# Kernel optimization log

Hardware: AMD Instinct MI355X
Metric: run time of the kernel (lower is better)

The kernel has to match this reference:

```python
import jax, jax.numpy as jnp
import numpy as np

B, N, C = 16, 65536, 21          # batch, anchors, classes (class 0 = background)
TH_CONF = 0.05                   # confidence threshold
TH_IOU = 0.5                     # NMS IoU threshold
TOP_K = 200                      # candidates kept per (batch, class) before NMS
V0, V1 = 0.1, 0.2                # SSD box-coder variances


def setup_inputs() -> dict:
    key = jax.random.key(0)
    k1, k2, k3, k4 = jax.random.split(key, 4)
    conf = jax.random.normal(k1, (B, N, C), dtype=jnp.float32)
    loc = jax.random.normal(k2, (B, N, 4), dtype=jnp.float32)
    # anchors in center form (cx, cy, w, h), normalized coords
    cxcy = jax.random.uniform(k3, (N, 2), dtype=jnp.float32)
    wh = 0.02 + 0.2 * jax.random.uniform(k4, (N, 2), dtype=jnp.float32)
    anchors = jnp.concatenate([cxcy, wh], axis=-1)
    return {"conf": conf, "loc": loc, "anchors": anchors}


def _decode(anchors, loc):
    # SSD decode: anchors [N,4] center form, loc [B,N,4] offsets -> [B,N,4] xyxy
    a_xy, a_wh = anchors[:, :2], anchors[:, 2:]
    xy = a_xy + loc[..., :2] * V0 * a_wh
    wh = a_wh * jnp.exp(loc[..., 2:] * V1)
    return jnp.concatenate([xy - 0.5 * wh, xy + 0.5 * wh], axis=-1)


def _iou(boxes):
    # boxes [K,4] xyxy -> pairwise IoU [K,K]
    area = jnp.maximum(boxes[:, 2] - boxes[:, 0], 0.0) * jnp.maximum(boxes[:, 3] - boxes[:, 1], 0.0)
    lt = jnp.maximum(boxes[:, None, :2], boxes[None, :, :2])
    rb = jnp.minimum(boxes[:, None, 2:], boxes[None, :, 2:])
    wh = jnp.maximum(rb - lt, 0.0)
    inter = wh[..., 0] * wh[..., 1]
    union = area[:, None] + area[None, :] - inter
    return inter / jnp.maximum(union, 1e-9)


def _nms_keep(iou, valid):
    # greedy NMS over score-sorted candidates; valid = (score >= TH_CONF)
    K = iou.shape[0]
    idx = jnp.arange(K)

    def body(keep, xs):
        row, v, i = xs
        suppressed = jnp.any((row > TH_IOU) & keep & (idx < i))
        k = v & (~suppressed)
        return keep.at[i].set(k), 0

    keep, _ = jax.lax.scan(body, jnp.zeros((K,), dtype=bool), (iou, valid, idx))
    return keep


def reference(conf, loc, anchors):
    score = jax.nn.softmax(conf, axis=2)            # [B,N,C]
    boxes = _decode(anchors, loc)                   # [B,N,4]
    # skip background class 0 (cls_base = 1 for softmax classifier)
    cls_scores = jnp.swapaxes(score[..., 1:], 1, 2)  # [B,C-1,N]
    top_s, top_i = jax.lax.top_k(cls_scores, TOP_K)  # [B,C-1,K], sorted desc
    top_boxes = jax.vmap(lambda bx, ix: bx[ix])(boxes, top_i)  # [B,C-1,K,4]
    valid = top_s >= TH_CONF
    keep = jax.vmap(jax.vmap(lambda b, v: _nms_keep(_iou(b), v)))(top_boxes, valid)  # [B,C-1,K]
    out_boxes = jnp.where(keep[..., None], top_boxes, 0.0)
    out_scores = jnp.where(keep, top_s, 0.0)
    return jnp.concatenate([out_boxes, out_scores[..., None]], axis=-1)  # [B,C-1,K,5]
```

## Files before the change

### kernel.cpp

```cpp
#include <hip/hip_runtime.h>
#include <stdint.h>

#define NB     16
#define NANCH  65536
#define NC     21
#define NCLS   20
#define NCOL   (NB * NCLS)
#define TOPK   200
#define NBINS  1024
#define CAP    256
#define CAPCOL 4096
#define CAPFAST 2048
#define CNTSTRIDE 16

constexpr float TH      = 0.05f;
constexpr float TPRE    = 0.20f;
constexpr float SCALE20 = (float)NBINS / 0.80f;
constexpr float SCALE05 = (float)NBINS / 0.95f;

__device__ __forceinline__ int bin20(float s) {
  int b = (int)((s - 0.20f) * SCALE20);
  return b < 0 ? 0 : (b > NBINS - 1 ? NBINS - 1 : b);
}
__device__ __forceinline__ int bin05(float s) {
  int b = (int)((s - 0.05f) * SCALE05);
  return b < 0 ? 0 : (b > NBINS - 1 ? NBINS - 1 : b);
}

__device__ __forceinline__ unsigned long long shflx64(unsigned long long v, int m) {
  unsigned int lo = (unsigned int)v, hi = (unsigned int)(v >> 32);
  lo = __shfl_xor(lo, m);
  hi = __shfl_xor(hi, m);
  return ((unsigned long long)hi << 32) | lo;
}
__device__ __forceinline__ unsigned long long rl64(unsigned long long v, int lane) {
  unsigned int lo = __builtin_amdgcn_readlane((int)(unsigned int)v, lane);
  unsigned int hi = __builtin_amdgcn_readlane((int)(unsigned int)(v >> 32), lane);
  return ((unsigned long long)hi << 32) | lo;
}

__device__ __forceinline__ void softmax_tail(const float* x, float* e, float& S) {
  float m = x[0];
#pragma unroll
  for (int c = 1; c < NC; ++c) m = fmaxf(m, x[c]);
#pragma unroll
  for (int c = 0; c < NC; ++c) e[c] = expf(x[c] - m);
  float r0 = e[0] + e[8],  r1 = e[1] + e[9],  r2 = e[2] + e[10], r3 = e[3] + e[11];
  float r4 = e[4] + e[12], r5 = e[5] + e[13], r6 = e[6] + e[14], r7 = e[7] + e[15];
  S = ((r0 + r1) + (r2 + r3)) + ((r4 + r5) + (r6 + r7));
  S += e[16]; S += e[17]; S += e[18]; S += e[19]; S += e[20];
}

__global__ __launch_bounds__(256) void softmax_collect_kernel(
    const float* __restrict__ conf,
    unsigned int* __restrict__ cnt, unsigned long long* __restrict__ cand) {
  const int tid = threadIdx.x;
  __shared__ float ld[256 * NC];
  const float4* src = (const float4*)conf + (long long)blockIdx.x * 1344;
  float4* dst4 = (float4*)ld;
#pragma unroll
  for (int i = 0; i < 5; ++i) dst4[tid + i * 256] = src[tid + i * 256];
  if (tid < 64) dst4[tid + 1280] = src[tid + 1280];
  __syncthreads();

  const int a = blockIdx.x * 256 + tid;
  const int b = a >> 16;
  const int n = a & (NANCH - 1);
  float x[NC];
#pragma unroll
  for (int c = 0; c < NC; ++c) x[c] = ld[tid * NC + c];
  float e[NC], S;
  softmax_tail(x, e, S);
  const float t = TPRE * S;
  unsigned int takemask = 0;
#pragma unroll
  for (int c = 0; c < NCLS; ++c)
    if (e[c + 1] >= t) takemask |= (1u << c);

  __shared__ unsigned int wcnt[4][NCLS];
  __shared__ unsigned int wbase[4][NCLS];
  const int wave = tid >> 6, lane = tid & 63;
#pragma unroll
  for (int c = 0; c < NCLS; ++c) {
    unsigned long long m = __ballot((takemask >> c) & 1);
    if (lane == 0) wcnt[wave][c] = (unsigned int)__popcll(m);
  }
  __syncthreads();
  if (tid < NCLS) {
    const int c = tid;
    unsigned int t0 = wcnt[0][c], t1 = wcnt[1][c], t2 = wcnt[2][c], t3 = wcnt[3][c];
    unsigned int tot = t0 + t1 + t2 + t3;
    unsigned int base = tot ? atomicAdd(&cnt[(b * NCLS + c) * CNTSTRIDE], tot) : 0u;
    wbase[0][c] = base;
    wbase[1][c] = base + t0;
    wbase[2][c] = base + t0 + t1;
    wbase[3][c] = base + t0 + t1 + t2;
  }
  __syncthreads();
#pragma unroll
  for (int c = 0; c < NCLS; ++c) {
    bool take = (takemask >> c) & 1;
    unsigned long long m = __ballot(take);
    if (take) {
      float s = e[c + 1] / S;
      unsigned int off = wbase[wave][c] +
                         (unsigned int)__popcll(m & ((1ULL << lane) - 1));
      if (off < CAPCOL) {
        unsigned int key = __float_as_uint(s) | 0x80000000u;
        cand[(long long)(b * NCLS + c) * CAPCOL + off] =
            ((unsigned long long)(key ^ 0xFFFFFFFFu) << 32) |
            (unsigned long long)(unsigned int)n;
      }
    }
  }
}

__global__ __launch_bounds__(1024) void topk_nms_kernel(
    const unsigned long long* __restrict__ candg,
    const unsigned int* __restrict__ cnt,
    const float* __restrict__ conf, const float* __restrict__ loc,
    const float* __restrict__ anchors, float* __restrict__ out) {
  const int bc = blockIdx.x;
  const int b  = bc / NCLS;
  const int cls = bc % NCLS;
  const int tid = threadIdx.x;

  __shared__ unsigned int hist[NBINS];
  __shared__ unsigned int part[256];
  __shared__ int s_sel, s_n;
  __shared__ unsigned long long cand[CAP];
  __shared__ float4 box4[TOPK];
  __shared__ float sscore[TOPK];
  __shared__ unsigned long long adj[TOPK][4];
  __shared__ unsigned long long keptw[4];

  int nc = (int)cnt[bc * CNTSTRIDE];
  const bool fast = (nc >= TOPK && nc <= CAPFAST);
  for (int i = tid; i < NBINS; i += 1024) hist[i] = 0;
  if (tid == 0) s_n = 0;
  __syncthreads();

  const unsigned long long* cg = candg + (long long)bc * CAPCOL;
  if (fast) {
    for (int i = tid; i < nc; i += 1024) {
      unsigned int key = (unsigned int)(cg[i] >> 32) ^ 0xFFFFFFFFu;
      float s = __uint_as_float(key ^ 0x80000000u);
      atomicAdd(&hist[bin20(s)], 1u);
    }
  } else {
    for (int n = tid; n < NANCH; n += 1024) {
      const float* row = conf + ((long long)b * NANCH + n) * NC;
      float x[NC], e[NC], S;
#pragma unroll
      for (int c = 0; c < NC; ++c) x[c] = row[c];
      softmax_tail(x, e, S);
      float s = e[cls + 1] / S;
      if (s >= TH) atomicAdd(&hist[bin05(s)], 1u);
    }
  }
  __syncthreads();

  if (tid < 256)
    part[tid] = hist[tid*4] + hist[tid*4+1] + hist[tid*4+2] + hist[tid*4+3];
  if (tid == 0) s_sel = -1;
  __syncthreads();
  if (tid < 64) {
    unsigned int p4 = part[tid*4] + part[tid*4+1] + part[tid*4+2] + part[tid*4+3];
    unsigned int sfx = p4;
#pragma unroll
    for (int off = 1; off < 64; off <<= 1) {
      unsigned int o = __shfl_down(sfx, off);
      if (tid + off < 64) sfx += o;
    }
    unsigned int above = sfx - p4;
    if (above < TOPK && sfx >= TOPK) {
      unsigned int cum = above; int sel = tid * 16; bool found = false;
      for (int q = 3; q >= 0 && !found; --q) {
        unsigned int pc = part[tid*4 + q];
        if (cum + pc >= TOPK) {
          for (int i = 3; i >= 0; --i) {
            unsigned int c = hist[(tid*4+q)*4 + i];
            if (cum + c >= TOPK) { sel = (tid*4+q)*4 + i; found = true; break; }
            cum += c;
          }
        } else cum += pc;
      }
      s_sel = sel;
    }
  }
  __syncthreads();
  const int sel = s_sel;

  if (fast) {
    for (int i = tid; i < nc; i += 1024) {
      unsigned long long k64 = cg[i];
      unsigned int key = (unsigned int)(k64 >> 32) ^ 0xFFFFFFFFu;
      float s = __uint_as_float(key ^ 0x80000000u);
      if (bin20(s) >= sel) {
        int pos = atomicAdd(&s_n, 1);
        if (pos < CAP) cand[pos] = k64;
      }
    }
  } else {
    for (int n = tid; n < NANCH; n += 1024) {
      const float* row = conf + ((long long)b * NANCH + n) * NC;
      float x[NC], e[NC], S;
#pragma unroll
      for (int c = 0; c < NC; ++c) x[c] = row[c];
      softmax_tail(x, e, S);
      float s = e[cls + 1] / S;
      if (s >= TH && (sel < 0 || bin05(s) >= sel)) {
        int pos = atomicAdd(&s_n, 1);
        if (pos < CAP) {
          unsigned int key = __float_as_uint(s) | 0x80000000u;
          cand[pos] = ((unsigned long long)(key ^ 0xFFFFFFFFu) << 32) |
                      (unsigned long long)(unsigned int)n;
        }
      }
    }
  }
  __syncthreads();
  int ncand = s_n; if (ncand > CAP) ncand = CAP;

  unsigned long long v = (tid < ncand) ? cand[tid] : ~0ULL;
  for (int k = 2; k <= CAP; k <<= 1) {
    const bool up = ((tid & k) == 0);
    for (int j = k >> 1; j >= 64; j >>= 1) {
      if (tid < 256) cand[tid] = v;
      __syncthreads();
      if (tid < 256) {
        unsigned long long o = cand[tid ^ j];
        bool keepMin = (((tid & j) == 0) == up);
        v = ((v < o) == keepMin) ? v : o;
      }
      __syncthreads();
    }
    if (tid < 256) {
      for (int j = (k >> 1) < 32 ? (k >> 1) : 32; j >= 1; j >>= 1) {
        unsigned long long o = shflx64(v, j);
        bool keepMin = (((tid & j) == 0) == up);
        v = ((v < o) == keepMin) ? v : o;
      }
    }
  }
  const int nsel = (ncand < TOPK) ? ncand : TOPK;

  if (tid < TOPK) {
    if (tid < nsel) {
      unsigned int key = (unsigned int)(v >> 32) ^ 0xFFFFFFFFu;
      float s = __uint_as_float(key ^ 0x80000000u);
      int idx = (int)(unsigned int)(v & 0xFFFFFFFFu);
      float4 anc = ((const float4*)anchors)[idx];
      float4 l   = ((const float4*)loc)[(long long)b * NANCH + idx];
      float cx = anc.x + (l.x * 0.1f) * anc.z;
      float cy = anc.y + (l.y * 0.1f) * anc.w;
      float w  = anc.z * expf(l.z * 0.2f);
      float h  = anc.w * expf(l.w * 0.2f);
      box4[tid] = make_float4(cx - 0.5f * w, cy - 0.5f * h,
                              cx + 0.5f * w, cy + 0.5f * h);
      sscore[tid] = s;
    } else {
      box4[tid] = make_float4(0.f, 0.f, 0.f, 0.f);
      sscore[tid] = 0.0f;
    }
  }
  __syncthreads();

  if (tid < TOPK * 4) {
    const int row = tid >> 2, w = tid & 3;
    const float4 a4 = box4[row];
    const float aar = fmaxf(a4.z - a4.x, 0.f) * fmaxf(a4.w - a4.y, 0.f);
    const int jend = (w < 3) ? 64 : (TOPK - 192);
    unsigned long long roww = 0;
#pragma unroll 4
    for (int jj = 0; jj < jend; ++jj) {
      const int j = (w << 6) + jj;
      float4 b4 = box4[j];
      float jar = fmaxf(b4.z - b4.x, 0.f) * fmaxf(b4.w - b4.y, 0.f);
      float ltx = fmaxf(a4.x, b4.x);
      float lty = fmaxf(a4.y, b4.y);
      float rbx = fminf(a4.z, b4.z);
      float rby = fminf(a4.w, b4.w);
      float iw = fmaxf(rbx - ltx, 0.0f);
      float ih = fmaxf(rby - lty, 0.0f);
      float inter = iw * ih;
      float uni = aar + jar - inter;
      float um = fmaxf(uni, 1e-9f);
      float half = 0.5f * um;
      bool hit;
      if (inter > half * 1.000001f)      hit = true;
      else if (inter < half * 0.999999f) hit = false;
      else                               hit = (inter / um > 0.5f);
      roww |= (unsigned long long)(hit ? 1u : 0u) << jj;
    }
    const int myw = row >> 6, myb = row & 63;
    unsigned long long tri = (w < myw) ? 0ULL
                           : (w > myw) ? ~0ULL
                           : ((myb == 63) ? 0ULL : (~0ULL << (myb + 1)));
    adj[row][w] = roww & tri;
  }
  __syncthreads();

  if (tid < 64) {
    const int l = tid;
    unsigned long long r0[4], r1[4], r2[4], r3[4];
#pragma unroll
    for (int w = 0; w < 4; ++w) {
      r0[w] = adj[l][w];
      r1[w] = adj[l + 64][w];
      r2[w] = adj[l + 128][w];
      r3[w] = (l < 8) ? adj[l + 192][w] : 0ULL;
    }
    unsigned long long sup0 = 0, sup1 = 0, sup2 = 0, sup3 = 0;
    unsigned long long k0 = 0, k1 = 0, k2 = 0, k3 = 0;
#pragma unroll 1
    for (int ii = 0; ii < 64; ++ii) {
      unsigned long long live = ((~sup0 >> ii) & 1ULL) &
                                (unsigned long long)(ii < nsel);
      unsigned long long mask = 0ULL - live;
      k0 |= live << ii;
      sup0 |= rl64(r0[0], ii) & mask; sup1 |= rl64(r0[1], ii) & mask;
      sup2 |= rl64(r0[2], ii) & mask; sup3 |= rl64(r0[3], ii) & mask;
    }
#pragma unroll 1
    for (int ii = 0; ii < 64; ++ii) {
      unsigned long long live = ((~sup1 >> ii) & 1ULL) &
                                (unsigned long long)((64 + ii) < nsel);
      unsigned long long mask = 0ULL - live;
      k1 |= live << ii;
      sup1 |= rl64(r1[1], ii) & mask; sup2 |= rl64(r1[2], ii) & mask;
      sup3 |= rl64(r1[3], ii) & mask;
    }
#pragma unroll 1
    for (int ii = 0; ii < 64; ++ii) {
      unsigned long long live = ((~sup2 >> ii) & 1ULL) &
                                (unsigned long long)((128 + ii) < nsel);
      unsigned long long mask = 0ULL - live;
      k2 |= live << ii;
      sup2 |= rl64(r2[2], ii) & mask; sup3 |= rl64(r2[3], ii) & mask;
    }
#pragma unroll 1
    for (int ii = 0; ii < 8; ++ii) {
      unsigned long long live = ((~sup3 >> ii) & 1ULL) &
                                (unsigned long long)((192 + ii) < nsel);
      unsigned long long mask = 0ULL - live;
      k3 |= live << ii;
      sup3 |= rl64(r3[3], ii) & mask;
    }
    if (l == 0) { keptw[0] = k0; keptw[1] = k1; keptw[2] = k2; keptw[3] = k3; }
  }
  __syncthreads();

  const float* fb = (const float*)box4;
  float* ob = out + (long long)bc * (TOPK * 5);
  for (int pos = tid; pos < TOPK * 5; pos += 1024) {
    int row = pos / 5;
    int k5  = pos - row * 5;
    bool kp = (keptw[row >> 6] >> (row & 63)) & 1ULL;
    float val = (k5 == 4) ? sscore[row] : fb[row * 4 + k5];
    ob[pos] = kp ? val : 0.0f;
  }
}

extern "C" void kernel_launch(void* const* d_in, const int* in_sizes, int n_in,
                              void* d_out, int out_size, void* d_ws, size_t ws_size,
                              hipStream_t stream) {
  const float* conf    = (const float*)d_in[0];
  const float* loc     = (const float*)d_in[1];
  const float* anchors = (const float*)d_in[2];
  float* out = (float*)d_out;

  char* ws = (char*)d_ws;
  unsigned long long* cand = (unsigned long long*)ws;
  unsigned int*       cnt  = (unsigned int*)(ws + 10485760);

  hipMemsetAsync(ws + 10485760, 0, 320 * CNTSTRIDE * 4, stream);
  softmax_collect_kernel<<<(NB * NANCH) / 256, 256, 0, stream>>>(conf, cnt, cand);
  topk_nms_kernel<<<NCOL, 1024, 0, stream>>>(cand, cnt, conf, loc, anchors, out);
}
```

Before: 92.10 us.

## Replace bitonic sort with rank-by-count and use wave-aggregated candidate appends

```diff
diff --git a/kernel.cpp b/kernel.cpp
--- a/kernel.cpp
+++ b/kernel.cpp
@@ -27,12 +27,6 @@
   return b < 0 ? 0 : (b > NBINS - 1 ? NBINS - 1 : b);
 }
 
-__device__ __forceinline__ unsigned long long shflx64(unsigned long long v, int m) {
-  unsigned int lo = (unsigned int)v, hi = (unsigned int)(v >> 32);
-  lo = __shfl_xor(lo, m);
-  hi = __shfl_xor(hi, m);
-  return ((unsigned long long)hi << 32) | lo;
-}
 __device__ __forceinline__ unsigned long long rl64(unsigned long long v, int lane) {
   unsigned int lo = __builtin_amdgcn_readlane((int)(unsigned int)v, lane);
   unsigned int hi = __builtin_amdgcn_readlane((int)(unsigned int)(v >> 32), lane);
@@ -124,6 +118,7 @@
   const int b  = bc / NCLS;
   const int cls = bc % NCLS;
   const int tid = threadIdx.x;
+  const int lane = tid & 63;
 
   __shared__ unsigned int hist[NBINS];
   __shared__ unsigned int part[256];
@@ -137,6 +132,8 @@
   int nc = (int)cnt[bc * CNTSTRIDE];
   const bool fast = (nc >= TOPK && nc <= CAPFAST);
   for (int i = tid; i < NBINS; i += 1024) hist[i] = 0;
+  if (tid < CAP) cand[tid] = ~0ULL;
+  if (tid < TOPK) { box4[tid] = make_float4(0.f,0.f,0.f,0.f); sscore[tid] = 0.f; }
   if (tid == 0) s_n = 0;
   __syncthreads();
 
@@ -192,76 +189,73 @@
   const int sel = s_sel;
 
   if (fast) {
-    for (int i = tid; i < nc; i += 1024) {
-      unsigned long long k64 = cg[i];
-      unsigned int key = (unsigned int)(k64 >> 32) ^ 0xFFFFFFFFu;
-      float s = __uint_as_float(key ^ 0x80000000u);
-      if (bin20(s) >= sel) {
-        int pos = atomicAdd(&s_n, 1);
+    const int ncr = (nc + 1023) & ~1023;
+    for (int i = tid; i < ncr; i += 1024) {
+      bool have = i < nc;
+      unsigned long long k64 = have ? cg[i] : 0ULL;
+      bool takeit = false;
+      if (have) {
+        unsigned int key = (unsigned int)(k64 >> 32) ^ 0xFFFFFFFFu;
+        float s = __uint_as_float(key ^ 0x80000000u);
+        takeit = bin20(s) >= sel;
+      }
+      unsigned long long m = __ballot(takeit);
+      int cw = (int)__popcll(m);
+      int base = 0;
+      if (lane == 0 && cw) base = atomicAdd(&s_n, cw);
+      base = __shfl(base, 0);
+      if (takeit) {
+        int pos = base + (int)__popcll(m & ((1ULL << lane) - 1));
         if (pos < CAP) cand[pos] = k64;
       }
     }
   } else {
-    for (int n = tid; n < NANCH; n += 1024) {
-      const float* row = conf + ((long long)b * NANCH + n) * NC;
+    for (int n0 = tid; n0 < NANCH; n0 += 1024) {
+      const float* row = conf + ((long long)b * NANCH + n0) * NC;
       float x[NC], e[NC], S;
 #pragma unroll
       for (int c = 0; c < NC; ++c) x[c] = row[c];
       softmax_tail(x, e, S);
       float s = e[cls + 1] / S;
-      if (s >= TH && (sel < 0 || bin05(s) >= sel)) {
-        int pos = atomicAdd(&s_n, 1);
+      bool takeit = (s >= TH && (sel < 0 || bin05(s) >= sel));
+      unsigned long long m = __ballot(takeit);
+      int cw = (int)__popcll(m);
+      int base = 0;
+      if (lane == 0 && cw) base = atomicAdd(&s_n, cw);
+      base = __shfl(base, 0);
+      if (takeit) {
+        int pos = base + (int)__popcll(m & ((1ULL << lane) - 1));
         if (pos < CAP) {
           unsigned int key = __float_as_uint(s) | 0x80000000u;
           cand[pos] = ((unsigned long long)(key ^ 0xFFFFFFFFu) << 32) |
-                      (unsigned long long)(unsigned int)n;
+                      (unsigned long long)(unsigned int)n0;
         }
       }
     }
   }
   __syncthreads();
   int ncand = s_n; if (ncand > CAP) ncand = CAP;
-
-  unsigned long long v = (tid < ncand) ? cand[tid] : ~0ULL;
-  for (int k = 2; k <= CAP; k <<= 1) {
-    const bool up = ((tid & k) == 0);
-    for (int j = k >> 1; j >= 64; j >>= 1) {
-      if (tid < 256) cand[tid] = v;
-      __syncthreads();
-      if (tid < 256) {
-        unsigned long long o = cand[tid ^ j];
-        bool keepMin = (((tid & j) == 0) == up);
-        v = ((v < o) == keepMin) ? v : o;
-      }
-      __syncthreads();
-    }
-    if (tid < 256) {
-      for (int j = (k >> 1) < 32 ? (k >> 1) : 32; j >= 1; j >>= 1) {
-        unsigned long long o = shflx64(v, j);
-        bool keepMin = (((tid & j) == 0) == up);
-        v = ((v < o) == keepMin) ? v : o;
-      }
-    }
-  }
   const int nsel = (ncand < TOPK) ? ncand : TOPK;
 
-  if (tid < TOPK) {
-    if (tid < nsel) {
-      unsigned int key = (unsigned int)(v >> 32) ^ 0xFFFFFFFFu;
+  if (tid < CAP && tid < ncand) {
+    const unsigned long long key64 = cand[tid];
+    int rank = 0;
+#pragma unroll 8
+    for (int j = 0; j < CAP; ++j)
+      rank += (cand[j] < key64) ? 1 : 0;
+    if (rank < TOPK) {
+      unsigned int key = (unsigned int)(key64 >> 32) ^ 0xFFFFFFFFu;
       float s = __uint_as_float(key ^ 0x80000000u);
-      int idx = (int)(unsigned int)(v & 0xFFFFFFFFu);
+      int idx = (int)(unsigned int)(key64 & 0xFFFFFFFFu);
       float4 anc = ((const float4*)anchors)[idx];
       float4 l   = ((const float4*)loc)[(long long)b * NANCH + idx];
       float cx = anc.x + (l.x * 0.1f) * anc.z;
       float cy = anc.y + (l.y * 0.1f) * anc.w;
       float w  = anc.z * expf(l.z * 0.2f);
       float h  = anc.w * expf(l.w * 0.2f);
-      box4[tid] = make_float4(cx - 0.5f * w, cy - 0.5f * h,
-                              cx + 0.5f * w, cy + 0.5f * h);
-      sscore[tid] = s;
-    } else {
-      box4[tid] = make_float4(0.f, 0.f, 0.f, 0.f);
-      sscore[tid] = 0.0f;
+      box4[rank] = make_float4(cx - 0.5f * w, cy - 0.5f * h,
+                               cx + 0.5f * w, cy + 0.5f * h);
+      sscore[rank] = s;
     }
   }
   __syncthreads();
```

After: 94.14 us. +2.2%, slower.
